# Kernel optimization log

Measured on AMD Instinct MI355X. Metric: run time of the kernel, lower is better.

## Reference

```python
import jax, jax.numpy as jnp
import numpy as np

H = 1024        # hidden_size
E = 16          # n_routed_experts
K = 4           # num_experts_per_tok (top_k)
I = 512         # moe_intermediate_size
NS = 2          # n_shared_experts
IS = I * NS     # shared-expert intermediate size
N = 2048        # num_tokens
ROUTED_SCALE = 2.5  # routed_scaling_factor


def setup_inputs() -> dict:
    key = jax.random.key(0)
    ks = jax.random.split(key, 6)
    s = 0.02
    return {
        "hidden_states": jax.random.normal(ks[0], (N, H), jnp.float32),
        "gate_w": jax.random.normal(ks[1], (H, E), jnp.float32) * s,
        "w_gate_up": jax.random.normal(ks[2], (E, H, 2 * I), jnp.float32) * s,
        "w_down": jax.random.normal(ks[3], (E, I, H), jnp.float32) * s,
        "shared_gate_up": jax.random.normal(ks[4], (H, 2 * IS), jnp.float32) * s,
        "shared_down": jax.random.normal(ks[5], (IS, H), jnp.float32) * s,
    }


def _moe_forward(x, gate_w, w_gate_up, w_down, shared_gate_up, shared_down):
    n = x.shape[0]
    # --- router: sigmoid scoring + top-k (num_expert_group=topk_group=1) ---
    router_logits = x @ gate_w                      # [N, E]
    scores = jax.nn.sigmoid(router_logits)
    top_vals, top_idx = jax.lax.top_k(scores, K)    # [N, K]
    # renormalize (norm_topk_prob=True)
    top_w = top_vals / jnp.sum(top_vals, axis=-1, keepdims=True)
    # dense combine weights [N, E], zero outside top-k
    w_dense = jnp.zeros((n, E), x.dtype).at[jnp.arange(n)[:, None], top_idx].add(top_w)

    # --- routed experts: SwiGLU per expert, weighted combine ---
    gu = jnp.einsum("nh,ehf->nef", x, w_gate_up)    # [N, E, 2I]
    act = jax.nn.silu(gu[..., :I]) * gu[..., I:]    # SiluAndMul -> [N, E, I]
    routed = jnp.einsum("nei,eih,ne->nh", act, w_down, w_dense)  # [N, H]

    # --- shared experts MLP (WBLMLP) ---
    gus = x @ shared_gate_up                        # [N, 2*IS]
    shared = (jax.nn.silu(gus[:, :IS]) * gus[:, IS:]) @ shared_down  # [N, H]

    return routed * ROUTED_SCALE + shared


def reference(hidden_states, gate_w, w_gate_up, w_down, shared_gate_up, shared_down):
    return _moe_forward(hidden_states, gate_w, w_gate_up, w_down,
                        shared_gate_up, shared_down)
```

## Files before the change

kernel.cpp:

```cpp
#include <hip/hip_runtime.h>
#include <hip/hip_bf16.h>
#include <stdint.h>

#define NTOK 2048
#define HDIM 1024
#define NEXP 16
#define TOPK 4
#define IR   512
#define ISH  1024
#define RSCALE 2.5f

typedef short bf16x4 __attribute__((ext_vector_type(4)));
typedef short bf16x8 __attribute__((ext_vector_type(8)));
typedef float f32x4  __attribute__((ext_vector_type(4)));

static __device__ __forceinline__ unsigned short f2bf(float f){
  union { float fv; uint32_t u; } v; v.fv = f;
  uint32_t r = v.u + 0x7fffu + ((v.u >> 16) & 1u);
  return (unsigned short)(r >> 16);
}
static __device__ __forceinline__ float bf2f(unsigned short s){
  union { uint32_t u; float f; } v; v.u = ((uint32_t)s) << 16;
  return v.f;
}
static __device__ __forceinline__ unsigned int pkbf2(float lo, float hi){
  union { __hip_bfloat162 b; unsigned int u; } cv;
  cv.b = __float22bfloat162_rn(make_float2(lo, hi));
  return cv.u;
}

__global__ __launch_bounds__(256) void router_kernel(
    const float* __restrict__ x, const float* __restrict__ gw,
    float* __restrict__ topkw, int* __restrict__ choice,
    unsigned short* __restrict__ xbf)
{
  __shared__ float sgw[NEXP][HDIM + 8];
  const int tid = threadIdx.x;
  for (int f = tid; f < HDIM * NEXP; f += 256){
    int i = f >> 4, e = f & 15;
    sgw[e][i] = gw[f];
  }
  __syncthreads();
  const int lane = tid & 63;
  const int t = blockIdx.x * 4 + (tid >> 6);

  float s[NEXP];
  #pragma unroll
  for (int e = 0; e < NEXP; e++) s[e] = 0.f;
  #pragma unroll
  for (int j = 0; j < 8; j++){
    const int off = 128 * j + lane * 2;
    float2 xv = *(const float2*)(x + (size_t)t * HDIM + off);
    ushort2 xs = { f2bf(xv.x), f2bf(xv.y) };
    *(ushort2*)(xbf + (size_t)t * HDIM + off) = xs;
    #pragma unroll
    for (int e = 0; e < NEXP; e++){
      float2 gv = *(const float2*)(&sgw[e][off]);
      s[e] += xv.x * gv.x + xv.y * gv.y;
    }
  }
  #pragma unroll
  for (int e = 0; e < NEXP; e++){
    #pragma unroll
    for (int off = 32; off; off >>= 1)
      s[e] += __shfl_xor(s[e], off);
  }
  float sc[NEXP];
  #pragma unroll
  for (int e = 0; e < NEXP; e++) sc[e] = 1.f / (1.f + __expf(-s[e]));

  unsigned mask = 0; float w[TOPK]; int id[TOPK];
  #pragma unroll
  for (int k = 0; k < TOPK; k++){
    float best = -1e30f; int bi = 0;
    #pragma unroll
    for (int e = 0; e < NEXP; e++){
      if (!((mask >> e) & 1u) && sc[e] > best){ best = sc[e]; bi = e; }
    }
    mask |= 1u << bi; id[k] = bi; w[k] = best;
  }
  float inv = 1.f / (w[0] + w[1] + w[2] + w[3]);
  if (lane == 0){
    #pragma unroll
    for (int k = 0; k < TOPK; k++){
      topkw[t * TOPK + k] = w[k] * inv;
      choice[t * TOPK + k] = id[k];
    }
  }
}

__global__ __launch_bounds__(256) void build_lists(
    const int* __restrict__ choice, int* __restrict__ counts, int* __restrict__ lists)
{
  const int e = blockIdx.x;
  const int tid = threadIdx.x;
  __shared__ int scnt[256];
  const int base = tid * 32;
  unsigned m = 0; int local = 0;
  #pragma unroll
  for (int i = 0; i < 32; i++){
    bool hit = (choice[base + i] == e);
    m |= (unsigned)hit << i;
    local += hit;
  }
  scnt[tid] = local;
  __syncthreads();
  int v = local;
  for (int off = 1; off < 256; off <<= 1){
    int add = (tid >= off) ? scnt[tid - off] : 0;
    __syncthreads();
    v += add; scnt[tid] = v;
    __syncthreads();
  }
  int pos = v - local;
  #pragma unroll
  for (int i = 0; i < 32; i++){
    if ((m >> i) & 1u) lists[e * NTOK + pos++] = base + i;
  }
  if (tid == 255) counts[e] = v;
}

__global__ __launch_bounds__(256) void gu_gemm(
    const unsigned short* __restrict__ xbf, const float* __restrict__ wgu,
    const float* __restrict__ sgu,
    unsigned short* __restrict__ act_r, unsigned short* __restrict__ act_s,
    const int* __restrict__ lists, const int* __restrict__ counts)
{
  __shared__ unsigned short sA[128 * 64];
  __shared__ unsigned short sB[128 * 64];
  __shared__ int sAid[128];

  const int tid = threadIdx.x;
  const int L = blockIdx.x;
  const bool routed = (L < 512);
  int e, mIdx, n0, count, NPAIR, NCH, LDB;
  const float* Bsrc;
  unsigned short* act;
  if (routed){
    e = L >> 5; int r = L & 31; mIdx = r >> 3; n0 = (r & 7) * 64;
    count = counts[e]; NPAIR = IR; NCH = 4; LDB = 2 * IR;
    Bsrc = wgu + (size_t)e * HDIM * (2 * IR);
    act = act_r;
  } else {
    int v = L - 512;
    e = 0; mIdx = v >> 4; n0 = (v & 15) * 64;
    count = NTOK; NPAIR = ISH; NCH = 16; LDB = 2 * ISH;
    Bsrc = sgu; act = act_s;
  }

  const int wv = tid >> 6, lane = tid & 63, lr = lane & 15, g = lane >> 4;
  const int wm = wv >> 1, wn = wv & 1;
  const int sw = lr >> 1;

  const int a = tid & 31, o = tid >> 5;
  const int alo = a & 15, aup = a >> 4;
  const int grp = ((alo >> 3) << 1) | aup;
  const int cbase = grp * 32 + 4 * (alo & 7);
  const int gcol = n0 + 4 * alo + (aup ? NPAIR : 0);
  const float* bthread = Bsrc + (size_t)(o * 8) * LDB + gcol;

  for (int mt = mIdx; mt * 128 < count; mt += NCH){
    const int m0 = mt * 128;
    __syncthreads();
    if (tid < 128){
      int idx = m0 + tid;
      int aid;
      if (routed) aid = (idx < count) ? lists[e * NTOK + idx] : lists[e * NTOK];
      else        aid = idx;
      sAid[tid] = aid;
    }
    __syncthreads();
    const unsigned short* asrc[4];
    unsigned short* adst[4];
    #pragma unroll
    for (int it = 0; it < 4; it++){
      int s = tid + it * 256;
      int row = s >> 3, j = s & 7;
      int aid = sAid[row];
      int tok = routed ? (aid >> 2) : aid;
      asrc[it] = xbf + (size_t)tok * HDIM + j * 8;
      adst[it] = sA + row * 64 + (j ^ ((row >> 1) & 7)) * 8;
    }

    const f32x4 z4 = {0.f, 0.f, 0.f, 0.f};
    f32x4 acc[4][4];
    #pragma unroll
    for (int i = 0; i < 4; i++)
      #pragma unroll
      for (int j = 0; j < 4; j++) acc[i][j] = z4;

    for (int k0 = 0; k0 < HDIM; k0 += 64){
      bf16x8 av[4];
      #pragma unroll
      for (int it = 0; it < 4; it++)
        av[it] = *(const bf16x8*)(asrc[it] + k0);
      #pragma unroll
      for (int it = 0; it < 4; it++)
        *(bf16x8*)adst[it] = av[it];
      float4 f[8];
      const float* bp = bthread + (size_t)k0 * LDB;
      #pragma unroll
      for (int r = 0; r < 8; r++)
        f[r] = *(const float4*)(bp + (size_t)r * LDB);
      #pragma unroll
      for (int i = 0; i < 4; i++){
        union { bf16x8 v; unsigned int u[4]; } pk;
        #pragma unroll
        for (int rp = 0; rp < 4; rp++){
          float lo = ((const float*)&f[2 * rp    ])[i];
          float hi = ((const float*)&f[2 * rp + 1])[i];
          pk.u[rp] = pkbf2(lo, hi);
        }
        int c = cbase + i;
        int pos = o ^ ((c >> 1) & 7);
        *(bf16x8*)(sB + c * 64 + pos * 8) = pk.v;
      }
      __syncthreads();
      #pragma unroll
      for (int h = 0; h < 2; h++){
        bf16x8 af[4], bfr[4];
        #pragma unroll
        for (int i = 0; i < 4; i++){
          int jx = ((h * 4 + g) ^ sw) * 8;
          af[i]  = *(const bf16x8*)(sA + (wm * 64 + i * 16 + lr) * 64 + jx);
          bfr[i] = *(const bf16x8*)(sB + (wn * 64 + i * 16 + lr) * 64 + jx);
        }
        #pragma unroll
        for (int mi = 0; mi < 4; mi++)
          #pragma unroll
          for (int ni = 0; ni < 4; ni++)
            acc[mi][ni] = __builtin_amdgcn_mfma_f32_16x16x32_bf16(af[mi], bfr[ni], acc[mi][ni], 0, 0, 0);
      }
      __syncthreads();
    }

    #pragma unroll
    for (int mi = 0; mi < 4; mi++){
      #pragma unroll
      for (int r = 0; r < 4; r++){
        int row = wm * 64 + mi * 16 + g * 4 + r;
        if (routed && m0 + row >= count) continue;
        int aid = sAid[row];
        size_t arow = (size_t)aid * NPAIR;
        #pragma unroll
        for (int ni = 0; ni < 2; ni++){
          float gv = acc[mi][ni][r];
          float uv = acc[mi][ni + 2][r];
          float av2 = gv / (1.f + __expf(-gv)) * uv;
          act[arow + n0 + wn * 32 + ni * 16 + lr] = f2bf(av2);
        }
      }
    }
  }
}

__global__ __launch_bounds__(256) void down_gemm(
    const unsigned short* __restrict__ act_r, const unsigned short* __restrict__ act_s,
    const float* __restrict__ wdn, const float* __restrict__ sdn,
    float* __restrict__ shout, unsigned short* __restrict__ downout,
    const int* __restrict__ lists, const int* __restrict__ counts)
{
  __shared__ unsigned short sA[128 * 64];
  __shared__ unsigned short sB[128 * 64];
  __shared__ int sAid[128];

  const int tid = threadIdx.x;
  const int L = blockIdx.x;
  const bool routed = (L < 512);
  int e, mIdx, n0, count, K, NCH;
  const float* Bsrc;
  const unsigned short* Ab;
  if (routed){
    e = L >> 5; int r = L & 31; mIdx = r >> 3; n0 = (r & 7) * 128;
    count = counts[e]; K = IR; NCH = 4;
    Bsrc = wdn + (size_t)e * IR * HDIM;
    Ab = act_r;
  } else {
    int v = L - 512;
    e = 0; mIdx = v >> 3; n0 = (v & 7) * 128;
    count = NTOK; K = ISH; NCH = 16;
    Bsrc = sdn; Ab = act_s;
  }

  const int wv = tid >> 6, lane = tid & 63, lr = lane & 15, g = lane >> 4;
  const int wm = wv >> 1, wn = wv & 1;
  const int sw = lr >> 1;

  const int a = tid & 31, o = tid >> 5;
  const int cbase = 4 * a;
  const float* bthread = Bsrc + (size_t)(o * 8) * HDIM + n0 + 4 * a;

  for (int mt = mIdx; mt * 128 < count; mt += NCH){
    const int m0 = mt * 128;
    __syncthreads();
    if (tid < 128){
      int idx = m0 + tid;
      int aid;
      if (routed) aid = (idx < count) ? lists[e * NTOK + idx] : lists[e * NTOK];
      else        aid = idx;
      sAid[tid] = aid;
    }
    __syncthreads();
    const unsigned short* asrc[4];
    unsigned short* adst[4];
    #pragma unroll
    for (int it = 0; it < 4; it++){
      int s = tid + it * 256;
      int row = s >> 3, j = s & 7;
      asrc[it] = Ab + (size_t)sAid[row] * K + j * 8;
      adst[it] = sA + row * 64 + (j ^ ((row >> 1) & 7)) * 8;
    }

    const f32x4 z4 = {0.f, 0.f, 0.f, 0.f};
    f32x4 acc[4][4];
    #pragma unroll
    for (int i = 0; i < 4; i++)
      #pragma unroll
      for (int j = 0; j < 4; j++) acc[i][j] = z4;

    for (int k0 = 0; k0 < K; k0 += 64){
      bf16x8 av[4];
      #pragma unroll
      for (int it = 0; it < 4; it++)
        av[it] = *(const bf16x8*)(asrc[it] + k0);
      #pragma unroll
      for (int it = 0; it < 4; it++)
        *(bf16x8*)adst[it] = av[it];
      float4 f[8];
      const float* bp = bthread + (size_t)k0 * HDIM;
      #pragma unroll
      for (int r = 0; r < 8; r++)
        f[r] = *(const float4*)(bp + (size_t)r * HDIM);
      #pragma unroll
      for (int i = 0; i < 4; i++){
        union { bf16x8 v; unsigned int u[4]; } pk;
        #pragma unroll
        for (int rp = 0; rp < 4; rp++){
          float lo = ((const float*)&f[2 * rp    ])[i];
          float hi = ((const float*)&f[2 * rp + 1])[i];
          pk.u[rp] = pkbf2(lo, hi);
        }
        int c = cbase + i;
        int pos = o ^ ((c >> 1) & 7);
        *(bf16x8*)(sB + c * 64 + pos * 8) = pk.v;
      }
      __syncthreads();
      #pragma unroll
      for (int h = 0; h < 2; h++){
        bf16x8 af[4], bfr[4];
        #pragma unroll
        for (int i = 0; i < 4; i++){
          int jx = ((h * 4 + g) ^ sw) * 8;
          af[i]  = *(const bf16x8*)(sA + (wm * 64 + i * 16 + lr) * 64 + jx);
          bfr[i] = *(const bf16x8*)(sB + (wn * 64 + i * 16 + lr) * 64 + jx);
        }
        #pragma unroll
        for (int mi = 0; mi < 4; mi++)
          #pragma unroll
          for (int ni = 0; ni < 4; ni++)
            acc[mi][ni] = __builtin_amdgcn_mfma_f32_16x16x32_bf16(af[mi], bfr[ni], acc[mi][ni], 0, 0, 0);
      }
      __syncthreads();
    }

    #pragma unroll
    for (int mi = 0; mi < 4; mi++){
      #pragma unroll
      for (int r = 0; r < 4; r++){
        int row = wm * 64 + mi * 16 + g * 4 + r;
        if (m0 + row >= count) continue;
        int aid = sAid[row];
        size_t orow = (size_t)aid * HDIM;
        if (routed){
          #pragma unroll
          for (int ni = 0; ni < 4; ni++)
            downout[orow + n0 + wn * 64 + ni * 16 + lr] = f2bf(acc[mi][ni][r]);
        } else {
          #pragma unroll
          for (int ni = 0; ni < 4; ni++)
            shout[orow + n0 + wn * 64 + ni * 16 + lr] = acc[mi][ni][r];
        }
      }
    }
  }
}

__global__ __launch_bounds__(256) void combine_kernel(
    float* __restrict__ out, const float* __restrict__ shout,
    const unsigned short* __restrict__ downout, const float* __restrict__ topkw)
{
  const int idx = blockIdx.x * 256 + threadIdx.x;
  const int t = idx >> 8;
  const int c4 = (idx & 255) * 4;
  float4 o = *(const float4*)(shout + (size_t)t * HDIM + c4);
  float r0 = 0.f, r1 = 0.f, r2 = 0.f, r3 = 0.f;
  #pragma unroll
  for (int k = 0; k < TOPK; k++){
    float w = topkw[t * TOPK + k];
    const ushort4 dv = *(const ushort4*)(downout + (size_t)(t * TOPK + k) * HDIM + c4);
    r0 += w * bf2f(dv.x); r1 += w * bf2f(dv.y);
    r2 += w * bf2f(dv.z); r3 += w * bf2f(dv.w);
  }
  o.x += RSCALE * r0; o.y += RSCALE * r1; o.z += RSCALE * r2; o.w += RSCALE * r3;
  *(float4*)(out + (size_t)t * HDIM + c4) = o;
}

extern "C" void kernel_launch(void* const* d_in, const int* in_sizes, int n_in,
                              void* d_out, int out_size, void* d_ws, size_t ws_size,
                              hipStream_t stream) {
  const float* x   = (const float*)d_in[0];
  const float* gw  = (const float*)d_in[1];
  const float* wgu = (const float*)d_in[2];
  const float* wdn = (const float*)d_in[3];
  const float* sgu = (const float*)d_in[4];
  const float* sdn = (const float*)d_in[5];
  float* out = (float*)d_out;

  char* ws = (char*)d_ws;
  float* topkw = (float*)(ws + 0);
  int* choice  = (int*)(ws + 32768);
  int* counts  = (int*)(ws + 65536);
  int* lists   = (int*)(ws + 65792);
  unsigned short* xbf     = (unsigned short*)(ws + 197120);
  unsigned short* act_r   = (unsigned short*)(ws + 197120 +  4194304ull);
  unsigned short* act_s   = (unsigned short*)(ws + 197120 + 12582912ull);
  unsigned short* downout = (unsigned short*)(ws + 197120 + 16777216ull);
  float*          shout   = (float*)(ws + 197120 + 33554432ull);

  router_kernel<<<NTOK / 4, 256, 0, stream>>>(x, gw, topkw, choice, xbf);
  build_lists<<<NEXP, 256, 0, stream>>>(choice, counts, lists);
  gu_gemm<<<768, 256, 0, stream>>>(xbf, wgu, sgu, act_r, act_s, lists, counts);
  down_gemm<<<640, 256, 0, stream>>>(act_r, act_s, wdn, sdn, shout, downout, lists, counts);
  combine_kernel<<<(NTOK * HDIM / 4) / 256, 256, 0, stream>>>(out, shout, downout, topkw);
}
```

Measured before the change: 130.4 us.

## Double GEMM M-tile to 256 rows with 512-thread blocks

```diff
diff --git a/kernel.cpp b/kernel.cpp
--- a/kernel.cpp
+++ b/kernel.cpp
@@ -120,31 +120,31 @@
   if (tid == 255) counts[e] = v;
 }
 
-__global__ __launch_bounds__(256) void gu_gemm(
+__global__ __launch_bounds__(512) void gu_gemm(
     const unsigned short* __restrict__ xbf, const float* __restrict__ wgu,
     const float* __restrict__ sgu,
     unsigned short* __restrict__ act_r, unsigned short* __restrict__ act_s,
     const int* __restrict__ lists, const int* __restrict__ counts)
 {
-  __shared__ unsigned short sA[128 * 64];
+  __shared__ unsigned short sA[256 * 64];
   __shared__ unsigned short sB[128 * 64];
-  __shared__ int sAid[128];
+  __shared__ int sAid[256];
 
   const int tid = threadIdx.x;
   const int L = blockIdx.x;
-  const bool routed = (L < 512);
+  const bool routed = (L < 256);
   int e, mIdx, n0, count, NPAIR, NCH, LDB;
   const float* Bsrc;
   unsigned short* act;
   if (routed){
-    e = L >> 5; int r = L & 31; mIdx = r >> 3; n0 = (r & 7) * 64;
-    count = counts[e]; NPAIR = IR; NCH = 4; LDB = 2 * IR;
+    e = L >> 4; int r = L & 15; mIdx = r >> 3; n0 = (r & 7) * 64;
+    count = counts[e]; NPAIR = IR; NCH = 2; LDB = 2 * IR;
     Bsrc = wgu + (size_t)e * HDIM * (2 * IR);
     act = act_r;
   } else {
-    int v = L - 512;
+    int v = L - 256;
     e = 0; mIdx = v >> 4; n0 = (v & 15) * 64;
-    count = NTOK; NPAIR = ISH; NCH = 16; LDB = 2 * ISH;
+    count = NTOK; NPAIR = ISH; NCH = 8; LDB = 2 * ISH;
     Bsrc = sgu; act = act_s;
   }
 
@@ -152,17 +152,17 @@
   const int wm = wv >> 1, wn = wv & 1;
   const int sw = lr >> 1;
 
-  const int a = tid & 31, o = tid >> 5;
+  const int a = tid & 31, o2 = tid >> 5;
   const int alo = a & 15, aup = a >> 4;
   const int grp = ((alo >> 3) << 1) | aup;
   const int cbase = grp * 32 + 4 * (alo & 7);
   const int gcol = n0 + 4 * alo + (aup ? NPAIR : 0);
-  const float* bthread = Bsrc + (size_t)(o * 8) * LDB + gcol;
-
-  for (int mt = mIdx; mt * 128 < count; mt += NCH){
-    const int m0 = mt * 128;
-    __syncthreads();
-    if (tid < 128){
+  const float* bthread = Bsrc + (size_t)(o2 * 4) * LDB + gcol;
+
+  for (int mt = mIdx; mt * 256 < count; mt += NCH){
+    const int m0 = mt * 256;
+    __syncthreads();
+    if (tid < 256){
       int idx = m0 + tid;
       int aid;
       if (routed) aid = (idx < count) ? lists[e * NTOK + idx] : lists[e * NTOK];
@@ -174,7 +174,7 @@
     unsigned short* adst[4];
     #pragma unroll
     for (int it = 0; it < 4; it++){
-      int s = tid + it * 256;
+      int s = tid + it * 512;
       int row = s >> 3, j = s & 7;
       int aid = sAid[row];
       int tok = routed ? (aid >> 2) : aid;
@@ -197,23 +197,19 @@
       #pragma unroll
       for (int it = 0; it < 4; it++)
         *(bf16x8*)adst[it] = av[it];
-      float4 f[8];
+      float4 f[4];
       const float* bp = bthread + (size_t)k0 * LDB;
       #pragma unroll
-      for (int r = 0; r < 8; r++)
+      for (int r = 0; r < 4; r++)
         f[r] = *(const float4*)(bp + (size_t)r * LDB);
       #pragma unroll
       for (int i = 0; i < 4; i++){
-        union { bf16x8 v; unsigned int u[4]; } pk;
-        #pragma unroll
-        for (int rp = 0; rp < 4; rp++){
-          float lo = ((const float*)&f[2 * rp    ])[i];
-          float hi = ((const float*)&f[2 * rp + 1])[i];
-          pk.u[rp] = pkbf2(lo, hi);
-        }
+        union { bf16x4 v; unsigned int u[2]; } pk;
+        pk.u[0] = pkbf2(((const float*)&f[0])[i], ((const float*)&f[1])[i]);
+        pk.u[1] = pkbf2(((const float*)&f[2])[i], ((const float*)&f[3])[i]);
         int c = cbase + i;
-        int pos = o ^ ((c >> 1) & 7);
-        *(bf16x8*)(sB + c * 64 + pos * 8) = pk.v;
+        int slot = o2 ^ ((((c >> 1) & 7)) << 1);
+        *(bf16x4*)(sB + c * 64 + slot * 4) = pk.v;
       }
       __syncthreads();
       #pragma unroll
@@ -254,31 +250,31 @@
   }
 }
 
-__global__ __launch_bounds__(256) void down_gemm(
+__global__ __launch_bounds__(512) void down_gemm(
     const unsigned short* __restrict__ act_r, const unsigned short* __restrict__ act_s,
     const float* __restrict__ wdn, const float* __restrict__ sdn,
     float* __restrict__ shout, unsigned short* __restrict__ downout,
     const int* __restrict__ lists, const int* __restrict__ counts)
 {
-  __shared__ unsigned short sA[128 * 64];
+  __shared__ unsigned short sA[256 * 64];
   __shared__ unsigned short sB[128 * 64];
-  __shared__ int sAid[128];
+  __shared__ int sAid[256];
 
   const int tid = threadIdx.x;
   const int L = blockIdx.x;
-  const bool routed = (L < 512);
+  const bool routed = (L < 256);
   int e, mIdx, n0, count, K, NCH;
   const float* Bsrc;
   const unsigned short* Ab;
   if (routed){
-    e = L >> 5; int r = L & 31; mIdx = r >> 3; n0 = (r & 7) * 128;
-    count = counts[e]; K = IR; NCH = 4;
+    e = L >> 4; int r = L & 15; mIdx = r >> 3; n0 = (r & 7) * 128;
+    count = counts[e]; K = IR; NCH = 2;
     Bsrc = wdn + (size_t)e * IR * HDIM;
     Ab = act_r;
   } else {
-    int v = L - 512;
+    int v = L - 256;
     e = 0; mIdx = v >> 3; n0 = (v & 7) * 128;
-    count = NTOK; K = ISH; NCH = 16;
+    count = NTOK; K = ISH; NCH = 8;
     Bsrc = sdn; Ab = act_s;
   }
 
@@ -286,14 +282,14 @@
   const int wm = wv >> 1, wn = wv & 1;
   const int sw = lr >> 1;
 
-  const int a = tid & 31, o = tid >> 5;
+  const int a = tid & 31, o2 = tid >> 5;
   const int cbase = 4 * a;
-  const float* bthread = Bsrc + (size_t)(o * 8) * HDIM + n0 + 4 * a;
-
-  for (int mt = mIdx; mt * 128 < count; mt += NCH){
-    const int m0 = mt * 128;
-    __syncthreads();
-    if (tid < 128){
+  const float* bthread = Bsrc + (size_t)(o2 * 4) * HDIM + n0 + 4 * a;
+
+  for (int mt = mIdx; mt * 256 < count; mt += NCH){
+    const int m0 = mt * 256;
+    __syncthreads();
+    if (tid < 256){
       int idx = m0 + tid;
       int aid;
       if (routed) aid = (idx < count) ? lists[e * NTOK + idx] : lists[e * NTOK];
@@ -305,7 +301,7 @@
     unsigned short* adst[4];
     #pragma unroll
     for (int it = 0; it < 4; it++){
-      int s = tid + it * 256;
+      int s = tid + it * 512;
       int row = s >> 3, j = s & 7;
       asrc[it] = Ab + (size_t)sAid[row] * K + j * 8;
       adst[it] = sA + row * 64 + (j ^ ((row >> 1) & 7)) * 8;
@@ -326,23 +322,19 @@
       #pragma unroll
       for (int it = 0; it < 4; it++)
         *(bf16x8*)adst[it] = av[it];
-      float4 f[8];
+      float4 f[4];
       const float* bp = bthread + (size_t)k0 * HDIM;
       #pragma unroll
-      for (int r = 0; r < 8; r++)
+      for (int r = 0; r < 4; r++)
         f[r] = *(const float4*)(bp + (size_t)r * HDIM);
       #pragma unroll
       for (int i = 0; i < 4; i++){
-        union { bf16x8 v; unsigned int u[4]; } pk;
-        #pragma unroll
-        for (int rp = 0; rp < 4; rp++){
-          float lo = ((const float*)&f[2 * rp    ])[i];
-          float hi = ((const float*)&f[2 * rp + 1])[i];
-          pk.u[rp] = pkbf2(lo, hi);
-        }
+        union { bf16x4 v; unsigned int u[2]; } pk;
+        pk.u[0] = pkbf2(((const float*)&f[0])[i], ((const float*)&f[1])[i]);
+        pk.u[1] = pkbf2(((const float*)&f[2])[i], ((const float*)&f[3])[i]);
         int c = cbase + i;
-        int pos = o ^ ((c >> 1) & 7);
-        *(bf16x8*)(sB + c * 64 + pos * 8) = pk.v;
+        int slot = o2 ^ ((((c >> 1) & 7)) << 1);
+        *(bf16x4*)(sB + c * 64 + slot * 4) = pk.v;
       }
       __syncthreads();
       #pragma unroll
@@ -429,7 +421,7 @@
 
   router_kernel<<<NTOK / 4, 256, 0, stream>>>(x, gw, topkw, choice, xbf);
   build_lists<<<NEXP, 256, 0, stream>>>(choice, counts, lists);
-  gu_gemm<<<768, 256, 0, stream>>>(xbf, wgu, sgu, act_r, act_s, lists, counts);
-  down_gemm<<<640, 256, 0, stream>>>(act_r, act_s, wdn, sdn, shout, downout, lists, counts);
+  gu_gemm<<<384, 512, 0, stream>>>(xbf, wgu, sgu, act_r, act_s, lists, counts);
+  down_gemm<<<320, 512, 0, stream>>>(act_r, act_s, wdn, sdn, shout, downout, lists, counts);
   combine_kernel<<<(NTOK * HDIM / 4) / 256, 256, 0, stream>>>(out, shout, downout, topkw);
 }
```

Measured after the change: 165.0 us. 26.5% more time.
